# Performance work log

Hardware: AMD Instinct MI355X
Metric: run time of the kernel (lower is better)

Reference implementation:

```python
import jax, jax.numpy as jnp
import numpy as np

B, M, A = 16384, 1024, 512
SETTLING_STEPS = 10
TAU = 0.1


def setup_inputs() -> dict:
    key = jax.random.key(0)
    k0, k1, k2 = jax.random.split(key, 3)
    x = jax.random.normal(k0, (B, M), dtype=jnp.float32)
    # input_proj: Linear(micro_dim, attractor_dim) -> weight (A, M), bias (A)
    W_in = jax.random.normal(k1, (A, M), dtype=jnp.float32) * (1.0 / np.sqrt(M))
    b_in = jnp.zeros((A,), dtype=jnp.float32)
    # J: orthogonal-init * 0.9 in original; here a scaled random matrix keeps
    # spectral radius moderate so tanh does not fully saturate (same math).
    J = jax.random.normal(k2, (A, A), dtype=jnp.float32) * (0.09 / np.sqrt(A))
    return {"x": x, "W_in": W_in, "b_in": b_in, "J": J}


def reference(x, W_in, b_in, J):
    tau = max(TAU, 1e-6)
    # drive = input_proj(x), computed once outside the settling loop
    drive = x @ W_in.T + b_in  # [B, A]
    sigma0 = jnp.zeros((x.shape[0], J.shape[0]), dtype=x.dtype)

    def step(sigma, _):
        # recurrent = F.linear(sigma, J) / tau; sigma = tanh(drive + recurrent)
        sigma = jnp.tanh(drive + (sigma @ J.T) * (1.0 / tau))
        return sigma, None

    sigma, _ = jax.lax.scan(step, sigma0, None, length=SETTLING_STEPS)
    return sigma
```

## Files before the change

kernel.cpp:

```cpp
#include <hip/hip_runtime.h>
#include <stdint.h>


#define B_DIM 16384
#define M_DIM 1024
#define A_DIM 512

typedef short bf16x8 __attribute__((ext_vector_type(8)));
typedef float f32x4 __attribute__((ext_vector_type(4)));

__device__ __forceinline__ unsigned short f2bf(float f) {
  unsigned int u = __float_as_uint(f);
  unsigned int r = (u + 0x7FFFu + ((u >> 16) & 1u)) >> 16;
  return (unsigned short)r;
}
__device__ __forceinline__ float bf2f(unsigned short s) {
  return __uint_as_float(((unsigned int)s) << 16);
}
__device__ __forceinline__ float fast_tanh(float x) {
  float t = __expf(2.0f * x);
  return fmaf(-2.0f, __builtin_amdgcn_rcpf(t + 1.0f), 1.0f);
}

__global__ void split_kernel(const float* __restrict__ src,
                             unsigned short* __restrict__ hi,
                             unsigned short* __restrict__ lo,
                             int n, float scale) {
  int i = blockIdx.x * 256 + threadIdx.x;
  if (i < n) {
    float v = src[i] * scale;
    unsigned short h = f2bf(v);
    hi[i] = h;
    lo[i] = f2bf(v - bf2f(h));
  }
}

__global__ __launch_bounds__(256) void drive_kernel(
    const float* __restrict__ x, const unsigned short* __restrict__ Whi,
    const unsigned short* __restrict__ Wlo, const float* __restrict__ bias,
    float* __restrict__ drive, unsigned short* __restrict__ sig) {
  __shared__ __align__(16) unsigned short Ah[128][40];
  __shared__ __align__(16) unsigned short Al[128][40];
  __shared__ __align__(16) unsigned short Bh[128][40];
  __shared__ __align__(16) unsigned short Bl[128][40];

  const int t = threadIdx.x;
  const int bm = blockIdx.y, bn = blockIdx.x;
  const int row = t >> 1, half = t & 1;
  const int lane = t & 63, wave = t >> 6;
  const int wm = wave >> 1, wn = wave & 1;
  const int quad = lane >> 4, l16 = lane & 15;

  f32x4 acc[4][4] = {};

  const float* xp = x + (size_t)(bm * 128 + row) * M_DIM + half * 16;
  const unsigned short* wh = Whi + (size_t)(bn * 128 + row) * M_DIM + half * 16;
  const unsigned short* wl = Wlo + (size_t)(bn * 128 + row) * M_DIM + half * 16;

  for (int k0 = 0; k0 < M_DIM; k0 += 32) {
    float4 v[4];
#pragma unroll
    for (int q = 0; q < 4; ++q) v[q] = *(const float4*)(xp + k0 + 4 * q);
    unsigned short hiv[16], lov[16];
#pragma unroll
    for (int q = 0; q < 4; ++q) {
      float fv[4] = {v[q].x, v[q].y, v[q].z, v[q].w};
#pragma unroll
      for (int e = 0; e < 4; ++e) {
        unsigned short h = f2bf(fv[e]);
        hiv[4 * q + e] = h;
        lov[4 * q + e] = f2bf(fv[e] - bf2f(h));
      }
    }
    *(uint4*)&Ah[row][half * 16]     = *(uint4*)&hiv[0];
    *(uint4*)&Ah[row][half * 16 + 8] = *(uint4*)&hiv[8];
    *(uint4*)&Al[row][half * 16]     = *(uint4*)&lov[0];
    *(uint4*)&Al[row][half * 16 + 8] = *(uint4*)&lov[8];
    *(uint4*)&Bh[row][half * 16]     = *(const uint4*)(wh + k0);
    *(uint4*)&Bh[row][half * 16 + 8] = *(const uint4*)(wh + k0 + 8);
    *(uint4*)&Bl[row][half * 16]     = *(const uint4*)(wl + k0);
    *(uint4*)&Bl[row][half * 16 + 8] = *(const uint4*)(wl + k0 + 8);
    __syncthreads();

    bf16x8 ah[4], al[4], bh[4], bl[4];
#pragma unroll
    for (int i = 0; i < 4; ++i) {
      ah[i] = *(const bf16x8*)&Ah[wm * 64 + i * 16 + l16][quad * 8];
      al[i] = *(const bf16x8*)&Al[wm * 64 + i * 16 + l16][quad * 8];
    }
#pragma unroll
    for (int j = 0; j < 4; ++j) {
      bh[j] = *(const bf16x8*)&Bh[wn * 64 + j * 16 + l16][quad * 8];
      bl[j] = *(const bf16x8*)&Bl[wn * 64 + j * 16 + l16][quad * 8];
    }
#pragma unroll
    for (int i = 0; i < 4; ++i)
#pragma unroll
      for (int j = 0; j < 4; ++j) {
        acc[i][j] = __builtin_amdgcn_mfma_f32_16x16x32_bf16(ah[i], bh[j], acc[i][j], 0, 0, 0);
        acc[i][j] = __builtin_amdgcn_mfma_f32_16x16x32_bf16(ah[i], bl[j], acc[i][j], 0, 0, 0);
        acc[i][j] = __builtin_amdgcn_mfma_f32_16x16x32_bf16(al[i], bh[j], acc[i][j], 0, 0, 0);
      }
    __syncthreads();
  }

#pragma unroll
  for (int i = 0; i < 4; ++i)
#pragma unroll
    for (int j = 0; j < 4; ++j) {
      int gcol = bn * 128 + wn * 64 + j * 16 + l16;
      float bv = bias[gcol];
#pragma unroll
      for (int r = 0; r < 4; ++r) {
        int grow = bm * 128 + wm * 64 + i * 16 + quad * 4 + r;
        float dv = acc[i][j][r] + bv;
        size_t idx = (size_t)grow * A_DIM + gcol;
        drive[idx] = dv;
        sig[idx] = f2bf(fast_tanh(dv));
      }
    }
}

__global__ __launch_bounds__(256) void step_kernel(
    const unsigned short* __restrict__ sin_, const unsigned short* __restrict__ Jhi,
    const unsigned short* __restrict__ Jlo, const float* __restrict__ drive,
    unsigned short* __restrict__ sout, float* __restrict__ outf, int last) {
  __shared__ __align__(16) unsigned short As[128][40];
  __shared__ __align__(16) unsigned short Bh[128][40];
  __shared__ __align__(16) unsigned short Bl[128][40];

  const int t = threadIdx.x;
  const int bm = blockIdx.y, bn = blockIdx.x;
  const int row = t >> 1, half = t & 1;
  const int lane = t & 63, wave = t >> 6;
  const int wm = wave >> 1, wn = wave & 1;
  const int quad = lane >> 4, l16 = lane & 15;

  f32x4 acc[4][4] = {};

  const unsigned short* ap = sin_ + (size_t)(bm * 128 + row) * A_DIM + half * 16;
  const unsigned short* jh = Jhi + (size_t)(bn * 128 + row) * A_DIM + half * 16;
  const unsigned short* jl = Jlo + (size_t)(bn * 128 + row) * A_DIM + half * 16;

  for (int k0 = 0; k0 < A_DIM; k0 += 32) {
    *(uint4*)&As[row][half * 16]     = *(const uint4*)(ap + k0);
    *(uint4*)&As[row][half * 16 + 8] = *(const uint4*)(ap + k0 + 8);
    *(uint4*)&Bh[row][half * 16]     = *(const uint4*)(jh + k0);
    *(uint4*)&Bh[row][half * 16 + 8] = *(const uint4*)(jh + k0 + 8);
    *(uint4*)&Bl[row][half * 16]     = *(const uint4*)(jl + k0);
    *(uint4*)&Bl[row][half * 16 + 8] = *(const uint4*)(jl + k0 + 8);
    __syncthreads();

    bf16x8 av[4], bh[4], bl[4];
#pragma unroll
    for (int i = 0; i < 4; ++i)
      av[i] = *(const bf16x8*)&As[wm * 64 + i * 16 + l16][quad * 8];
#pragma unroll
    for (int j = 0; j < 4; ++j) {
      bh[j] = *(const bf16x8*)&Bh[wn * 64 + j * 16 + l16][quad * 8];
      bl[j] = *(const bf16x8*)&Bl[wn * 64 + j * 16 + l16][quad * 8];
    }
#pragma unroll
    for (int i = 0; i < 4; ++i)
#pragma unroll
      for (int j = 0; j < 4; ++j) {
        acc[i][j] = __builtin_amdgcn_mfma_f32_16x16x32_bf16(av[i], bh[j], acc[i][j], 0, 0, 0);
        acc[i][j] = __builtin_amdgcn_mfma_f32_16x16x32_bf16(av[i], bl[j], acc[i][j], 0, 0, 0);
      }
    __syncthreads();
  }

#pragma unroll
  for (int i = 0; i < 4; ++i)
#pragma unroll
    for (int j = 0; j < 4; ++j) {
      int gcol = bn * 128 + wn * 64 + j * 16 + l16;
#pragma unroll
      for (int r = 0; r < 4; ++r) {
        int grow = bm * 128 + wm * 64 + i * 16 + quad * 4 + r;
        size_t idx = (size_t)grow * A_DIM + gcol;
        float v = fast_tanh(drive[idx] + acc[i][j][r]);
        if (last) outf[idx] = v;
        else sout[idx] = f2bf(v);
      }
    }
}

extern "C" void kernel_launch(void* const* d_in, const int* in_sizes, int n_in,
                              void* d_out, int out_size, void* d_ws, size_t ws_size,
                              hipStream_t stream) {
  const float* x = (const float*)d_in[0];
  const float* W = (const float*)d_in[1];
  const float* b = (const float*)d_in[2];
  const float* J = (const float*)d_in[3];
  float* out = (float*)d_out;

  char* ws = (char*)d_ws;
  float* drive         = (float*)(ws);
  unsigned short* sigA = (unsigned short*)(ws + 33554432);
  unsigned short* sigB = (unsigned short*)(ws + 50331648);
  unsigned short* Whi  = (unsigned short*)(ws + 67108864);
  unsigned short* Wlo  = (unsigned short*)(ws + 68157440);
  unsigned short* Jhi  = (unsigned short*)(ws + 69206016);
  unsigned short* Jlo  = (unsigned short*)(ws + 69730304);

  const int nW = A_DIM * M_DIM;
  const int nJ = A_DIM * A_DIM;
  split_kernel<<<(nW + 255) / 256, 256, 0, stream>>>(W, Whi, Wlo, nW, 1.0f);
  split_kernel<<<(nJ + 255) / 256, 256, 0, stream>>>(J, Jhi, Jlo, nJ, 10.0f);

  dim3 grid(A_DIM / 128, B_DIM / 128);
  drive_kernel<<<grid, 256, 0, stream>>>(x, Whi, Wlo, b, drive, sigA);

  unsigned short* cur = sigA;
  unsigned short* nxt = sigB;
  for (int s = 0; s < 9; ++s) {
    step_kernel<<<grid, 256, 0, stream>>>(cur, Jhi, Jlo, drive, nxt, out, s == 8);
    unsigned short* tmp = cur; cur = nxt; nxt = tmp;
  }
}
```

Measured before the change: 562.5 us.

## Use direct global-to-LDS loads with XOR swizzle and K=64 tiles in step kernel

The step kernel now stages sigma and the J hi/lo tiles with global_load_lds, which writes straight from global memory into shared memory without passing through registers. The shared tiles are 64-wide in K with an XOR swizzle on 16-byte chunks to avoid bank conflicts, which halves the number of K iterations and barriers. This costs more LDS per block (48KB), which may lower occupancy, and it relies on the exact lane-to-LDS address pattern of the builtin.

```diff
diff --git a/kernel.cpp b/kernel.cpp
--- a/kernel.cpp
+++ b/kernel.cpp
@@ -8,6 +8,11 @@
 
 typedef short bf16x8 __attribute__((ext_vector_type(8)));
 typedef float f32x4 __attribute__((ext_vector_type(4)));
+
+#define GLDS16(g, l)                                                        \
+  __builtin_amdgcn_global_load_lds(                                         \
+      (const __attribute__((address_space(1))) unsigned int*)(g),           \
+      (__attribute__((address_space(3))) unsigned int*)(l), 16, 0, 0)
 
 __device__ __forceinline__ unsigned short f2bf(float f) {
   unsigned int u = __float_as_uint(f);
@@ -125,48 +130,58 @@
     const unsigned short* __restrict__ sin_, const unsigned short* __restrict__ Jhi,
     const unsigned short* __restrict__ Jlo, const float* __restrict__ drive,
     unsigned short* __restrict__ sout, float* __restrict__ outf, int last) {
-  __shared__ __align__(16) unsigned short As[128][40];
-  __shared__ __align__(16) unsigned short Bh[128][40];
-  __shared__ __align__(16) unsigned short Bl[128][40];
+  __shared__ __align__(16) unsigned short As[128 * 64];
+  __shared__ __align__(16) unsigned short Bhs[128 * 64];
+  __shared__ __align__(16) unsigned short Bls[128 * 64];
 
   const int t = threadIdx.x;
   const int bm = blockIdx.y, bn = blockIdx.x;
-  const int row = t >> 1, half = t & 1;
   const int lane = t & 63, wave = t >> 6;
   const int wm = wave >> 1, wn = wave & 1;
   const int quad = lane >> 4, l16 = lane & 15;
+  const int rl = lane >> 3;
+  const int gsrc = (lane & 7) ^ rl;
 
   f32x4 acc[4][4] = {};
 
-  const unsigned short* ap = sin_ + (size_t)(bm * 128 + row) * A_DIM + half * 16;
-  const unsigned short* jh = Jhi + (size_t)(bn * 128 + row) * A_DIM + half * 16;
-  const unsigned short* jl = Jlo + (size_t)(bn * 128 + row) * A_DIM + half * 16;
-
-  for (int k0 = 0; k0 < A_DIM; k0 += 32) {
-    *(uint4*)&As[row][half * 16]     = *(const uint4*)(ap + k0);
-    *(uint4*)&As[row][half * 16 + 8] = *(const uint4*)(ap + k0 + 8);
-    *(uint4*)&Bh[row][half * 16]     = *(const uint4*)(jh + k0);
-    *(uint4*)&Bh[row][half * 16 + 8] = *(const uint4*)(jh + k0 + 8);
-    *(uint4*)&Bl[row][half * 16]     = *(const uint4*)(jl + k0);
-    *(uint4*)&Bl[row][half * 16 + 8] = *(const uint4*)(jl + k0 + 8);
-    __syncthreads();
-
-    bf16x8 av[4], bh[4], bl[4];
-#pragma unroll
-    for (int i = 0; i < 4; ++i)
-      av[i] = *(const bf16x8*)&As[wm * 64 + i * 16 + l16][quad * 8];
-#pragma unroll
-    for (int j = 0; j < 4; ++j) {
-      bh[j] = *(const bf16x8*)&Bh[wn * 64 + j * 16 + l16][quad * 8];
-      bl[j] = *(const bf16x8*)&Bl[wn * 64 + j * 16 + l16][quad * 8];
-    }
-#pragma unroll
-    for (int i = 0; i < 4; ++i)
+  const unsigned short* aT = sin_ + (size_t)(bm * 128) * A_DIM;
+  const unsigned short* bhT = Jhi + (size_t)(bn * 128) * A_DIM;
+  const unsigned short* blT = Jlo + (size_t)(bn * 128) * A_DIM;
+
+  for (int k0 = 0; k0 < A_DIM; k0 += 64) {
+#pragma unroll
+    for (int q = 0; q < 4; ++q) {
+      const int c = wave * 4 + q;
+      const size_t goff = (size_t)(c * 8 + rl) * A_DIM + k0 + gsrc * 8;
+      GLDS16(aT + goff, &As[c * 512]);
+      GLDS16(bhT + goff, &Bhs[c * 512]);
+      GLDS16(blT + goff, &Bls[c * 512]);
+    }
+    __syncthreads();
+
+#pragma unroll
+    for (int h = 0; h < 2; ++h) {
+      bf16x8 af[4], bhf[4], blf[4];
+#pragma unroll
+      for (int i = 0; i < 4; ++i) {
+        const int r = wm * 64 + i * 16 + l16;
+        af[i] = *(const bf16x8*)&As[r * 64 + 8 * ((4 * h + quad) ^ (r & 7))];
+      }
 #pragma unroll
       for (int j = 0; j < 4; ++j) {
-        acc[i][j] = __builtin_amdgcn_mfma_f32_16x16x32_bf16(av[i], bh[j], acc[i][j], 0, 0, 0);
-        acc[i][j] = __builtin_amdgcn_mfma_f32_16x16x32_bf16(av[i], bl[j], acc[i][j], 0, 0, 0);
-      }
+        const int r = wn * 64 + j * 16 + l16;
+        const int off = r * 64 + 8 * ((4 * h + quad) ^ (r & 7));
+        bhf[j] = *(const bf16x8*)&Bhs[off];
+        blf[j] = *(const bf16x8*)&Bls[off];
+      }
+#pragma unroll
+      for (int i = 0; i < 4; ++i)
+#pragma unroll
+        for (int j = 0; j < 4; ++j) {
+          acc[i][j] = __builtin_amdgcn_mfma_f32_16x16x32_bf16(af[i], bhf[j], acc[i][j], 0, 0, 0);
+          acc[i][j] = __builtin_amdgcn_mfma_f32_16x16x32_bf16(af[i], blf[j], acc[i][j], 0, 0, 0);
+        }
+    }
     __syncthreads();
   }
 
```

Result: faster. 520.1 us (-7.5%).

## Fuse drive GEMM and all settling steps into one persistent row-block kernel

Applied to the files above, without the earlier changes.

Replaces the drive kernel and nine step launches with a single kernel where each block owns 64 batch rows across all 512 attractor columns. The drive values stay in registers and sigma lives in XOR-swizzled shared memory across iterations, so the drive and sigma buffers no longer round-trip through global memory and nine launches disappear. W and J tiles are now read directly from global/L2 into registers with no LDS staging. The costs are heavy register pressure (acc plus drv, 256 floats per thread), 64KB of LDS per block limiting occupancy, and only 256 blocks in the grid.

```diff
diff --git a/kernel.cpp b/kernel.cpp
--- a/kernel.cpp
+++ b/kernel.cpp
@@ -35,155 +35,135 @@
   }
 }
 
-__global__ __launch_bounds__(256) void drive_kernel(
+__global__ __launch_bounds__(256) void fused_kernel(
     const float* __restrict__ x, const unsigned short* __restrict__ Whi,
     const unsigned short* __restrict__ Wlo, const float* __restrict__ bias,
-    float* __restrict__ drive, unsigned short* __restrict__ sig) {
-  __shared__ __align__(16) unsigned short Ah[128][40];
-  __shared__ __align__(16) unsigned short Al[128][40];
-  __shared__ __align__(16) unsigned short Bh[128][40];
-  __shared__ __align__(16) unsigned short Bl[128][40];
+    const unsigned short* __restrict__ Jhi, const unsigned short* __restrict__ Jlo,
+    float* __restrict__ out) {
+  __shared__ __align__(16) unsigned short sigL[64 * 512];
 
   const int t = threadIdx.x;
-  const int bm = blockIdx.y, bn = blockIdx.x;
-  const int row = t >> 1, half = t & 1;
-  const int lane = t & 63, wave = t >> 6;
-  const int wm = wave >> 1, wn = wave & 1;
+  const int bm = blockIdx.x;
+  const int lane = t & 63, w = t >> 6;
   const int quad = lane >> 4, l16 = lane & 15;
 
-  f32x4 acc[4][4] = {};
+  f32x4 acc[4][8];
+  float drv[4][8][4];
 
-  const float* xp = x + (size_t)(bm * 128 + row) * M_DIM + half * 16;
-  const unsigned short* wh = Whi + (size_t)(bn * 128 + row) * M_DIM + half * 16;
-  const unsigned short* wl = Wlo + (size_t)(bn * 128 + row) * M_DIM + half * 16;
+#pragma unroll
+  for (int i = 0; i < 4; ++i)
+#pragma unroll
+    for (int j = 0; j < 8; ++j) acc[i][j] = (f32x4){0.f, 0.f, 0.f, 0.f};
 
-  for (int k0 = 0; k0 < M_DIM; k0 += 32) {
-    float4 v[4];
+#pragma unroll 2
+  for (int c = 0; c < M_DIM / 32; ++c) {
+    bf16x8 xh[4], xl[4];
 #pragma unroll
-    for (int q = 0; q < 4; ++q) v[q] = *(const float4*)(xp + k0 + 4 * q);
-    unsigned short hiv[16], lov[16];
+    for (int i = 0; i < 4; ++i) {
+      const float* xp =
+          x + (size_t)(bm * 64 + i * 16 + l16) * M_DIM + c * 32 + quad * 8;
+      float4 a0 = *(const float4*)xp;
+      float4 a1 = *(const float4*)(xp + 4);
+      float fv[8] = {a0.x, a0.y, a0.z, a0.w, a1.x, a1.y, a1.z, a1.w};
 #pragma unroll
-    for (int q = 0; q < 4; ++q) {
-      float fv[4] = {v[q].x, v[q].y, v[q].z, v[q].w};
-#pragma unroll
-      for (int e = 0; e < 4; ++e) {
+      for (int e = 0; e < 8; ++e) {
         unsigned short h = f2bf(fv[e]);
-        hiv[4 * q + e] = h;
-        lov[4 * q + e] = f2bf(fv[e] - bf2f(h));
+        xh[i][e] = (short)h;
+        xl[i][e] = (short)f2bf(fv[e] - bf2f(h));
       }
     }
-    *(uint4*)&Ah[row][half * 16]     = *(uint4*)&hiv[0];
-    *(uint4*)&Ah[row][half * 16 + 8] = *(uint4*)&hiv[8];
-    *(uint4*)&Al[row][half * 16]     = *(uint4*)&lov[0];
-    *(uint4*)&Al[row][half * 16 + 8] = *(uint4*)&lov[8];
-    *(uint4*)&Bh[row][half * 16]     = *(const uint4*)(wh + k0);
-    *(uint4*)&Bh[row][half * 16 + 8] = *(const uint4*)(wh + k0 + 8);
-    *(uint4*)&Bl[row][half * 16]     = *(const uint4*)(wl + k0);
-    *(uint4*)&Bl[row][half * 16 + 8] = *(const uint4*)(wl + k0 + 8);
-    __syncthreads();
+#pragma unroll
+    for (int j = 0; j < 8; ++j) {
+      const size_t off =
+          (size_t)(w * 128 + j * 16 + l16) * M_DIM + c * 32 + quad * 8;
+      bf16x8 bh = *(const bf16x8*)(Whi + off);
+      bf16x8 bl = *(const bf16x8*)(Wlo + off);
+#pragma unroll
+      for (int i = 0; i < 4; ++i) {
+        acc[i][j] = __builtin_amdgcn_mfma_f32_16x16x32_bf16(xh[i], bh, acc[i][j], 0, 0, 0);
+        acc[i][j] = __builtin_amdgcn_mfma_f32_16x16x32_bf16(xl[i], bh, acc[i][j], 0, 0, 0);
+        acc[i][j] = __builtin_amdgcn_mfma_f32_16x16x32_bf16(xh[i], bl, acc[i][j], 0, 0, 0);
+      }
+    }
+  }
 
-    bf16x8 ah[4], al[4], bh[4], bl[4];
 #pragma unroll
-    for (int i = 0; i < 4; ++i) {
-      ah[i] = *(const bf16x8*)&Ah[wm * 64 + i * 16 + l16][quad * 8];
-      al[i] = *(const bf16x8*)&Al[wm * 64 + i * 16 + l16][quad * 8];
-    }
-#pragma unroll
-    for (int j = 0; j < 4; ++j) {
-      bh[j] = *(const bf16x8*)&Bh[wn * 64 + j * 16 + l16][quad * 8];
-      bl[j] = *(const bf16x8*)&Bl[wn * 64 + j * 16 + l16][quad * 8];
-    }
+  for (int j = 0; j < 8; ++j) {
+    float bv = bias[w * 128 + j * 16 + l16];
 #pragma unroll
     for (int i = 0; i < 4; ++i)
 #pragma unroll
-      for (int j = 0; j < 4; ++j) {
-        acc[i][j] = __builtin_amdgcn_mfma_f32_16x16x32_bf16(ah[i], bh[j], acc[i][j], 0, 0, 0);
-        acc[i][j] = __builtin_amdgcn_mfma_f32_16x16x32_bf16(ah[i], bl[j], acc[i][j], 0, 0, 0);
-        acc[i][j] = __builtin_amdgcn_mfma_f32_16x16x32_bf16(al[i], bh[j], acc[i][j], 0, 0, 0);
-      }
-    __syncthreads();
+      for (int r = 0; r < 4; ++r) drv[i][j][r] = acc[i][j][r] + bv;
   }
 
 #pragma unroll
   for (int i = 0; i < 4; ++i)
 #pragma unroll
-    for (int j = 0; j < 4; ++j) {
-      int gcol = bn * 128 + wn * 64 + j * 16 + l16;
-      float bv = bias[gcol];
+    for (int j = 0; j < 8; ++j)
 #pragma unroll
       for (int r = 0; r < 4; ++r) {
-        int grow = bm * 128 + wm * 64 + i * 16 + quad * 4 + r;
-        float dv = acc[i][j][r] + bv;
-        size_t idx = (size_t)grow * A_DIM + gcol;
-        drive[idx] = dv;
-        sig[idx] = f2bf(fast_tanh(dv));
+        int row = i * 16 + quad * 4 + r;
+        int col = w * 128 + j * 16 + l16;
+        int addr = row * 512 + (((col >> 3) ^ (row & 7)) << 3) + (col & 7);
+        sigL[addr] = f2bf(fast_tanh(drv[i][j][r]));
       }
-    }
-}
+  __syncthreads();
 
-__global__ __launch_bounds__(256) void step_kernel(
-    const unsigned short* __restrict__ sin_, const unsigned short* __restrict__ Jhi,
-    const unsigned short* __restrict__ Jlo, const float* __restrict__ drive,
-    unsigned short* __restrict__ sout, float* __restrict__ outf, int last) {
-  __shared__ __align__(16) unsigned short As[128][40];
-  __shared__ __align__(16) unsigned short Bh[128][40];
-  __shared__ __align__(16) unsigned short Bl[128][40];
-
-  const int t = threadIdx.x;
-  const int bm = blockIdx.y, bn = blockIdx.x;
-  const int row = t >> 1, half = t & 1;
-  const int lane = t & 63, wave = t >> 6;
-  const int wm = wave >> 1, wn = wave & 1;
-  const int quad = lane >> 4, l16 = lane & 15;
-
-  f32x4 acc[4][4] = {};
-
-  const unsigned short* ap = sin_ + (size_t)(bm * 128 + row) * A_DIM + half * 16;
-  const unsigned short* jh = Jhi + (size_t)(bn * 128 + row) * A_DIM + half * 16;
-  const unsigned short* jl = Jlo + (size_t)(bn * 128 + row) * A_DIM + half * 16;
-
-  for (int k0 = 0; k0 < A_DIM; k0 += 32) {
-    *(uint4*)&As[row][half * 16]     = *(const uint4*)(ap + k0);
-    *(uint4*)&As[row][half * 16 + 8] = *(const uint4*)(ap + k0 + 8);
-    *(uint4*)&Bh[row][half * 16]     = *(const uint4*)(jh + k0);
-    *(uint4*)&Bh[row][half * 16 + 8] = *(const uint4*)(jh + k0 + 8);
-    *(uint4*)&Bl[row][half * 16]     = *(const uint4*)(jl + k0);
-    *(uint4*)&Bl[row][half * 16 + 8] = *(const uint4*)(jl + k0 + 8);
-    __syncthreads();
-
-    bf16x8 av[4], bh[4], bl[4];
-#pragma unroll
-    for (int i = 0; i < 4; ++i)
-      av[i] = *(const bf16x8*)&As[wm * 64 + i * 16 + l16][quad * 8];
-#pragma unroll
-    for (int j = 0; j < 4; ++j) {
-      bh[j] = *(const bf16x8*)&Bh[wn * 64 + j * 16 + l16][quad * 8];
-      bl[j] = *(const bf16x8*)&Bl[wn * 64 + j * 16 + l16][quad * 8];
-    }
+  for (int s = 0; s < 9; ++s) {
 #pragma unroll
     for (int i = 0; i < 4; ++i)
 #pragma unroll
-      for (int j = 0; j < 4; ++j) {
-        acc[i][j] = __builtin_amdgcn_mfma_f32_16x16x32_bf16(av[i], bh[j], acc[i][j], 0, 0, 0);
-        acc[i][j] = __builtin_amdgcn_mfma_f32_16x16x32_bf16(av[i], bl[j], acc[i][j], 0, 0, 0);
-      }
-    __syncthreads();
-  }
+      for (int j = 0; j < 8; ++j) acc[i][j] = (f32x4){0.f, 0.f, 0.f, 0.f};
 
 #pragma unroll
-  for (int i = 0; i < 4; ++i)
+    for (int c = 0; c < A_DIM / 32; ++c) {
+      bf16x8 af[4];
 #pragma unroll
-    for (int j = 0; j < 4; ++j) {
-      int gcol = bn * 128 + wn * 64 + j * 16 + l16;
+      for (int i = 0; i < 4; ++i)
+        af[i] = *(const bf16x8*)&sigL[(i * 16 + l16) * 512 +
+                                      (((c * 4 + quad) ^ (l16 & 7)) << 3)];
 #pragma unroll
-      for (int r = 0; r < 4; ++r) {
-        int grow = bm * 128 + wm * 64 + i * 16 + quad * 4 + r;
-        size_t idx = (size_t)grow * A_DIM + gcol;
-        float v = fast_tanh(drive[idx] + acc[i][j][r]);
-        if (last) outf[idx] = v;
-        else sout[idx] = f2bf(v);
+      for (int j = 0; j < 8; ++j) {
+        const size_t off =
+            (size_t)(w * 128 + j * 16 + l16) * A_DIM + c * 32 + quad * 8;
+        bf16x8 bh = *(const bf16x8*)(Jhi + off);
+        bf16x8 bl = *(const bf16x8*)(Jlo + off);
+#pragma unroll
+        for (int i = 0; i < 4; ++i) {
+          acc[i][j] = __builtin_amdgcn_mfma_f32_16x16x32_bf16(af[i], bh, acc[i][j], 0, 0, 0);
+          acc[i][j] = __builtin_amdgcn_mfma_f32_16x16x32_bf16(af[i], bl, acc[i][j], 0, 0, 0);
+        }
       }
     }
+
+    if (s < 8) {
+      __syncthreads();
+#pragma unroll
+      for (int i = 0; i < 4; ++i)
+#pragma unroll
+        for (int j = 0; j < 8; ++j)
+#pragma unroll
+          for (int r = 0; r < 4; ++r) {
+            int row = i * 16 + quad * 4 + r;
+            int col = w * 128 + j * 16 + l16;
+            int addr = row * 512 + (((col >> 3) ^ (row & 7)) << 3) + (col & 7);
+            sigL[addr] = f2bf(fast_tanh(drv[i][j][r] + acc[i][j][r]));
+          }
+      __syncthreads();
+    } else {
+#pragma unroll
+      for (int i = 0; i < 4; ++i)
+#pragma unroll
+        for (int j = 0; j < 8; ++j)
+#pragma unroll
+          for (int r = 0; r < 4; ++r) {
+            int row = bm * 64 + i * 16 + quad * 4 + r;
+            int col = w * 128 + j * 16 + l16;
+            out[(size_t)row * A_DIM + col] =
+                fast_tanh(drv[i][j][r] + acc[i][j][r]);
+          }
+    }
+  }
 }
 
 extern "C" void kernel_launch(void* const* d_in, const int* in_sizes, int n_in,
@@ -196,26 +176,15 @@
   float* out = (float*)d_out;
 
   char* ws = (char*)d_ws;
-  float* drive         = (float*)(ws);
-  unsigned short* sigA = (unsigned short*)(ws + 33554432);
-  unsigned short* sigB = (unsigned short*)(ws + 50331648);
-  unsigned short* Whi  = (unsigned short*)(ws + 67108864);
-  unsigned short* Wlo  = (unsigned short*)(ws + 68157440);
-  unsigned short* Jhi  = (unsigned short*)(ws + 69206016);
-  unsigned short* Jlo  = (unsigned short*)(ws + 69730304);
+  unsigned short* Whi = (unsigned short*)(ws);
+  unsigned short* Wlo = (unsigned short*)(ws + 1048576);
+  unsigned short* Jhi = (unsigned short*)(ws + 2097152);
+  unsigned short* Jlo = (unsigned short*)(ws + 2621440);
 
   const int nW = A_DIM * M_DIM;
   const int nJ = A_DIM * A_DIM;
   split_kernel<<<(nW + 255) / 256, 256, 0, stream>>>(W, Whi, Wlo, nW, 1.0f);
   split_kernel<<<(nJ + 255) / 256, 256, 0, stream>>>(J, Jhi, Jlo, nJ, 10.0f);
 
-  dim3 grid(A_DIM / 128, B_DIM / 128);
-  drive_kernel<<<grid, 256, 0, stream>>>(x, Whi, Wlo, b, drive, sigA);
-
-  unsigned short* cur = sigA;
-  unsigned short* nxt = sigB;
-  for (int s = 0; s < 9; ++s) {
-    step_kernel<<<grid, 256, 0, stream>>>(cur, Jhi, Jlo, drive, nxt, out, s == 8);
-    unsigned short* tmp = cur; cur = nxt; nxt = tmp;
-  }
+  fused_kernel<<<B_DIM / 64, 256, 0, stream>>>(x, Whi, Wlo, b, Jhi, Jlo, out);
 }
```

Result: slower. 1.389 ms (+147.0%).

## Fuse all settling steps into one persistent kernel keeping sigma in LDS

Applied to the files above, without the earlier changes.

Replaces the nine separate step kernel launches with a single settle kernel. Each 512-thread block owns 64 batch rows, keeps sigma in swizzled shared memory and the drive values in registers, and iterates all steps locally. J hi/lo fragments are read straight from global memory/L2 every step with no LDS staging. This removes the per-step global round trips of sigma and drive and the launch overhead. In exchange it uses heavy register pressure (drive values plus accumulators) and only 256 blocks, which may leave CUs underoccupied.

```diff
diff --git a/kernel.cpp b/kernel.cpp
--- a/kernel.cpp
+++ b/kernel.cpp
@@ -38,7 +38,7 @@
 __global__ __launch_bounds__(256) void drive_kernel(
     const float* __restrict__ x, const unsigned short* __restrict__ Whi,
     const unsigned short* __restrict__ Wlo, const float* __restrict__ bias,
-    float* __restrict__ drive, unsigned short* __restrict__ sig) {
+    float* __restrict__ drive) {
   __shared__ __align__(16) unsigned short Ah[128][40];
   __shared__ __align__(16) unsigned short Al[128][40];
   __shared__ __align__(16) unsigned short Bh[128][40];
@@ -113,77 +113,98 @@
 #pragma unroll
       for (int r = 0; r < 4; ++r) {
         int grow = bm * 128 + wm * 64 + i * 16 + quad * 4 + r;
-        float dv = acc[i][j][r] + bv;
-        size_t idx = (size_t)grow * A_DIM + gcol;
-        drive[idx] = dv;
-        sig[idx] = f2bf(fast_tanh(dv));
-      }
-    }
-}
-
-__global__ __launch_bounds__(256) void step_kernel(
-    const unsigned short* __restrict__ sin_, const unsigned short* __restrict__ Jhi,
-    const unsigned short* __restrict__ Jlo, const float* __restrict__ drive,
-    unsigned short* __restrict__ sout, float* __restrict__ outf, int last) {
-  __shared__ __align__(16) unsigned short As[128][40];
-  __shared__ __align__(16) unsigned short Bh[128][40];
-  __shared__ __align__(16) unsigned short Bl[128][40];
+        drive[(size_t)grow * A_DIM + gcol] = acc[i][j][r] + bv;
+      }
+    }
+}
+
+__global__ __launch_bounds__(512, 2) void settle_kernel(
+    const float* __restrict__ drive, const unsigned short* __restrict__ Jhi,
+    const unsigned short* __restrict__ Jlo, float* __restrict__ out) {
+  __shared__ __align__(16) unsigned short sigL[64 * 512];
 
   const int t = threadIdx.x;
-  const int bm = blockIdx.y, bn = blockIdx.x;
-  const int row = t >> 1, half = t & 1;
-  const int lane = t & 63, wave = t >> 6;
-  const int wm = wave >> 1, wn = wave & 1;
+  const int bm = blockIdx.x;
+  const int lane = t & 63, w = t >> 6;
   const int quad = lane >> 4, l16 = lane & 15;
 
-  f32x4 acc[4][4] = {};
-
-  const unsigned short* ap = sin_ + (size_t)(bm * 128 + row) * A_DIM + half * 16;
-  const unsigned short* jh = Jhi + (size_t)(bn * 128 + row) * A_DIM + half * 16;
-  const unsigned short* jl = Jlo + (size_t)(bn * 128 + row) * A_DIM + half * 16;
-
-  for (int k0 = 0; k0 < A_DIM; k0 += 32) {
-    *(uint4*)&As[row][half * 16]     = *(const uint4*)(ap + k0);
-    *(uint4*)&As[row][half * 16 + 8] = *(const uint4*)(ap + k0 + 8);
-    *(uint4*)&Bh[row][half * 16]     = *(const uint4*)(jh + k0);
-    *(uint4*)&Bh[row][half * 16 + 8] = *(const uint4*)(jh + k0 + 8);
-    *(uint4*)&Bl[row][half * 16]     = *(const uint4*)(jl + k0);
-    *(uint4*)&Bl[row][half * 16 + 8] = *(const uint4*)(jl + k0 + 8);
-    __syncthreads();
-
-    bf16x8 av[4], bh[4], bl[4];
+  float drv[4][4][4];
+  f32x4 acc[4][4];
+
+#pragma unroll
+  for (int i = 0; i < 4; ++i)
+#pragma unroll
+    for (int j = 0; j < 4; ++j) {
+      const int col = w * 64 + j * 16 + l16;
+#pragma unroll
+      for (int r = 0; r < 4; ++r) {
+        const int row = i * 16 + quad * 4 + r;
+        drv[i][j][r] = drive[(size_t)(bm * 64 + row) * A_DIM + col];
+        const int addr =
+            row * 512 + (((col >> 3) ^ (row & 7)) << 3) + (col & 7);
+        sigL[addr] = f2bf(fast_tanh(drv[i][j][r]));
+      }
+    }
+  __syncthreads();
+
+  for (int s = 0; s < 9; ++s) {
 #pragma unroll
     for (int i = 0; i < 4; ++i)
-      av[i] = *(const bf16x8*)&As[wm * 64 + i * 16 + l16][quad * 8];
-#pragma unroll
-    for (int j = 0; j < 4; ++j) {
-      bh[j] = *(const bf16x8*)&Bh[wn * 64 + j * 16 + l16][quad * 8];
-      bl[j] = *(const bf16x8*)&Bl[wn * 64 + j * 16 + l16][quad * 8];
-    }
-#pragma unroll
-    for (int i = 0; i < 4; ++i)
+#pragma unroll
+      for (int j = 0; j < 4; ++j) acc[i][j] = (f32x4){0.f, 0.f, 0.f, 0.f};
+
+#pragma unroll
+    for (int c = 0; c < A_DIM / 32; ++c) {
+      bf16x8 af[4];
+#pragma unroll
+      for (int i = 0; i < 4; ++i)
+        af[i] = *(const bf16x8*)&sigL[(i * 16 + l16) * 512 +
+                                      (((c * 4 + quad) ^ (l16 & 7)) << 3)];
 #pragma unroll
       for (int j = 0; j < 4; ++j) {
-        acc[i][j] = __builtin_amdgcn_mfma_f32_16x16x32_bf16(av[i], bh[j], acc[i][j], 0, 0, 0);
-        acc[i][j] = __builtin_amdgcn_mfma_f32_16x16x32_bf16(av[i], bl[j], acc[i][j], 0, 0, 0);
-      }
-    __syncthreads();
+        const size_t off =
+            (size_t)(w * 64 + j * 16 + l16) * A_DIM + c * 32 + quad * 8;
+        bf16x8 bh = *(const bf16x8*)(Jhi + off);
+        bf16x8 bl = *(const bf16x8*)(Jlo + off);
+#pragma unroll
+        for (int i = 0; i < 4; ++i) {
+          acc[i][j] = __builtin_amdgcn_mfma_f32_16x16x32_bf16(af[i], bh, acc[i][j], 0, 0, 0);
+          acc[i][j] = __builtin_amdgcn_mfma_f32_16x16x32_bf16(af[i], bl, acc[i][j], 0, 0, 0);
+        }
+      }
+    }
+
+    if (s < 8) {
+      __syncthreads();
+#pragma unroll
+      for (int i = 0; i < 4; ++i)
+#pragma unroll
+        for (int j = 0; j < 4; ++j) {
+          const int col = w * 64 + j * 16 + l16;
+#pragma unroll
+          for (int r = 0; r < 4; ++r) {
+            const int row = i * 16 + quad * 4 + r;
+            const int addr =
+                row * 512 + (((col >> 3) ^ (row & 7)) << 3) + (col & 7);
+            sigL[addr] = f2bf(fast_tanh(drv[i][j][r] + acc[i][j][r]));
+          }
+        }
+      __syncthreads();
+    } else {
+#pragma unroll
+      for (int i = 0; i < 4; ++i)
+#pragma unroll
+        for (int j = 0; j < 4; ++j) {
+          const int col = w * 64 + j * 16 + l16;
+#pragma unroll
+          for (int r = 0; r < 4; ++r) {
+            const int row = bm * 64 + i * 16 + quad * 4 + r;
+            out[(size_t)row * A_DIM + col] =
+                fast_tanh(drv[i][j][r] + acc[i][j][r]);
+          }
+        }
+    }
   }
-
-#pragma unroll
-  for (int i = 0; i < 4; ++i)
-#pragma unroll
-    for (int j = 0; j < 4; ++j) {
-      int gcol = bn * 128 + wn * 64 + j * 16 + l16;
-#pragma unroll
-      for (int r = 0; r < 4; ++r) {
-        int grow = bm * 128 + wm * 64 + i * 16 + quad * 4 + r;
-        size_t idx = (size_t)grow * A_DIM + gcol;
-        float v = fast_tanh(drive[idx] + acc[i][j][r]);
-        if (last) outf[idx] = v;
-        else sout[idx] = f2bf(v);
-      }
-    }
 }
 
 extern "C" void kernel_launch(void* const* d_in, const int* in_sizes, int n_in,
@@ -196,13 +217,11 @@
   float* out = (float*)d_out;
 
   char* ws = (char*)d_ws;
-  float* drive         = (float*)(ws);
-  unsigned short* sigA = (unsigned short*)(ws + 33554432);
-  unsigned short* sigB = (unsigned short*)(ws + 50331648);
-  unsigned short* Whi  = (unsigned short*)(ws + 67108864);
-  unsigned short* Wlo  = (unsigned short*)(ws + 68157440);
-  unsigned short* Jhi  = (unsigned short*)(ws + 69206016);
-  unsigned short* Jlo  = (unsigned short*)(ws + 69730304);
+  float* drive        = (float*)(ws);
+  unsigned short* Whi = (unsigned short*)(ws + 33554432);
+  unsigned short* Wlo = (unsigned short*)(ws + 34603008);
+  unsigned short* Jhi = (unsigned short*)(ws + 35651584);
+  unsigned short* Jlo = (unsigned short*)(ws + 36175872);
 
   const int nW = A_DIM * M_DIM;
   const int nJ = A_DIM * A_DIM;
@@ -210,12 +229,7 @@
   split_kernel<<<(nJ + 255) / 256, 256, 0, stream>>>(J, Jhi, Jlo, nJ, 10.0f);
 
   dim3 grid(A_DIM / 128, B_DIM / 128);
-  drive_kernel<<<grid, 256, 0, stream>>>(x, Whi, Wlo, b, drive, sigA);
-
-  unsigned short* cur = sigA;
-  unsigned short* nxt = sigB;
-  for (int s = 0; s < 9; ++s) {
-    step_kernel<<<grid, 256, 0, stream>>>(cur, Jhi, Jlo, drive, nxt, out, s == 8);
-    unsigned short* tmp = cur; cur = nxt; nxt = tmp;
-  }
-}
+  drive_kernel<<<grid, 256, 0, stream>>>(x, Whi, Wlo, b, drive);
+
+  settle_kernel<<<B_DIM / 64, 512, 0, stream>>>(drive, Jhi, Jlo, out);
+}
```

Result: slower. 1.028 ms (+82.8%).
